# Kernel optimization log

Hardware: AMD Instinct MI355X
Metric: run time of the kernel (lower is better)

The kernel has to match this reference:

```python
import jax, jax.numpy as jnp
import numpy as np

FP8_MAX = 448.0  # torch.finfo(torch.float8_e4m3fn).max

def per_tensor_quantize(t):
    amax = jnp.max(jnp.abs(t))
    scale = FP8_MAX / jnp.maximum(amax, 1e-12)
    q = jnp.clip(t * scale, -FP8_MAX, FP8_MAX).astype(jnp.float8_e4m3fn)
    return q, (1.0 / scale).astype(jnp.float32)

def fp8_gemm(q, a_scale, w_q, w_scale, out_dtype):
    # emulate: linear(A.to(out)*a_scale, B.to(out)*b_scale)
    A = q.astype(out_dtype) * a_scale
    B = w_q.astype(out_dtype) * w_scale
    return A @ B.T

def setup_inputs() -> dict:
    key = jax.random.key(0)
    k1, k2, k3, k4 = jax.random.split(key, 4)
    tokens, hidden, ffn = 4096, 4096, 10752
    return {
        "x": jax.random.normal(k1, (tokens, hidden), jnp.float32),
        "expert_w1": jax.random.normal(k2, (ffn, hidden), jnp.float32) * 0.02,
        "expert_v1": jax.random.normal(k3, (ffn, hidden), jnp.float32) * 0.02,
        "expert_w2": jax.random.normal(k4, (ffn, hidden), jnp.float32) * 0.02,
    }

def reference(x, expert_w1, expert_v1, expert_w2):
    dt = x.dtype
    # weight quantization (as done in _quantize_weights per expert)
    w1_q, w1_s = per_tensor_quantize(expert_w1)
    v1_q, v1_s = per_tensor_quantize(expert_v1)
    w2_q, w2_s = per_tensor_quantize(expert_w2)
    # activation quantization + gate/up GEMMs
    qin, x_s = per_tensor_quantize(x)
    gate = fp8_gemm(qin, x_s, w1_q, w1_s, dt)          # [N, ffn]
    up = fp8_gemm(qin, x_s, v1_q, v1_s, dt)            # [N, ffn]
    inter = jax.nn.silu(gate) * up                      # fused GLU
    qmid, m_s = per_tensor_quantize(inter)
    # down proj uses expert_w2.t() -> B = [hidden, ffn]
    down = fp8_gemm(qmid, m_s, w2_q.T, w2_s, dt)        # [N, hidden]
    return down
```

## Files before the change

### kernel.cpp

```cpp
#include <hip/hip_runtime.h>
#include <cstdint>
#include <cstddef>

typedef float f32x4 __attribute__((ext_vector_type(4)));
typedef float f32x16 __attribute__((ext_vector_type(16)));
typedef int i32x4 __attribute__((ext_vector_type(4)));
typedef int i32x8 __attribute__((ext_vector_type(8)));
typedef unsigned char u8;

static __device__ __forceinline__ void gload_lds16(const void* g, void* l) {
  __builtin_amdgcn_global_load_lds(
      (__attribute__((address_space(1))) void*)(void*)g,
      (__attribute__((address_space(3))) void*)l,
      16, 0, 0);
}

#if defined(__has_builtin)
#if __has_builtin(__builtin_amdgcn_cvt_pk_fp8_f32)
#define HAVE_HW_FP8 1
#endif
#endif

__device__ __forceinline__ u8 f32_to_e4m3_sw(float x) {
  unsigned s = (__float_as_uint(x) >> 24) & 0x80;
  float ax = fabsf(x);
  if (!(ax > 0.0f)) return (u8)s;
  if (ax >= 448.0f) return (u8)(s | 0x7e);
  if (ax < 0.015625f) {
    int m = (int)rintf(ax * 512.0f);
    if (m >= 8) return (u8)(s | 0x08);
    return (u8)(s | m);
  }
  int e = ilogbf(ax);
  int m = (int)rintf(ldexpf(ax, 3 - e));
  if (m == 16) { ++e; m = 8; }
  return (u8)(s | ((e + 7) << 3) | (m - 8));
}

__device__ __forceinline__ unsigned cvt4_fp8(float a, float b, float c, float d) {
#ifdef HAVE_HW_FP8
  int lo = __builtin_amdgcn_cvt_pk_fp8_f32(a, b, 0, false);
  return (unsigned)__builtin_amdgcn_cvt_pk_fp8_f32(c, d, lo, true);
#else
  return (unsigned)f32_to_e4m3_sw(a) | ((unsigned)f32_to_e4m3_sw(b) << 8) |
         ((unsigned)f32_to_e4m3_sw(c) << 16) | ((unsigned)f32_to_e4m3_sw(d) << 24);
#endif
}

__global__ __launch_bounds__(256) void amax_kernel(const float* __restrict__ src, size_t n4,
                                                   unsigned* __restrict__ out) {
  float m = 0.0f;
  size_t stride = (size_t)gridDim.x * blockDim.x;
  const f32x4* p = (const f32x4*)src;
  for (size_t i = (size_t)blockIdx.x * blockDim.x + threadIdx.x; i < n4; i += stride) {
    f32x4 v = p[i];
    m = fmaxf(m, fmaxf(fmaxf(fabsf(v[0]), fabsf(v[1])), fmaxf(fabsf(v[2]), fabsf(v[3]))));
  }
#pragma unroll
  for (int off = 32; off > 0; off >>= 1) m = fmaxf(m, __shfl_down(m, off));
  __shared__ float red[4];
  int lane = threadIdx.x & 63, wid = threadIdx.x >> 6;
  if (lane == 0) red[wid] = m;
  __syncthreads();
  if (threadIdx.x == 0) {
    float v = fmaxf(fmaxf(red[0], red[1]), fmaxf(red[2], red[3]));
    atomicMax(out, __float_as_uint(v));
  }
}

__global__ __launch_bounds__(256) void quant_kernel(const float* __restrict__ src,
                                                    u8* __restrict__ dst,
                                                    const unsigned* __restrict__ amax_bits,
                                                    size_t n8) {
  float amax = __uint_as_float(*amax_bits);
  float scale = 448.0f / fmaxf(amax, 1e-12f);
  size_t stride = (size_t)gridDim.x * blockDim.x;
  const f32x4* p = (const f32x4*)src;
  uint2* q = (uint2*)dst;
  for (size_t i = (size_t)blockIdx.x * blockDim.x + threadIdx.x; i < n8; i += stride) {
    f32x4 a = p[2 * i], b = p[2 * i + 1];
    float a0 = fminf(fmaxf(a[0] * scale, -448.f), 448.f);
    float a1 = fminf(fmaxf(a[1] * scale, -448.f), 448.f);
    float a2 = fminf(fmaxf(a[2] * scale, -448.f), 448.f);
    float a3 = fminf(fmaxf(a[3] * scale, -448.f), 448.f);
    float b0 = fminf(fmaxf(b[0] * scale, -448.f), 448.f);
    float b1 = fminf(fmaxf(b[1] * scale, -448.f), 448.f);
    float b2 = fminf(fmaxf(b[2] * scale, -448.f), 448.f);
    float b3 = fminf(fmaxf(b[3] * scale, -448.f), 448.f);
    uint2 r;
    r.x = cvt4_fp8(a0, a1, a2, a3);
    r.y = cvt4_fp8(b0, b1, b2, b3);
    q[i] = r;
  }
}

__global__ __launch_bounds__(256) void quantT_kernel(const float* __restrict__ src,
                                                     u8* __restrict__ dst,
                                                     const unsigned* __restrict__ amax_bits,
                                                     int R, int C) {
  __shared__ float t[64][65];
  float amax = __uint_as_float(*amax_bits);
  float scale = 448.0f / fmaxf(amax, 1e-12f);
  int nbr = R >> 6;
  int br = (int)blockIdx.x % nbr, bc = (int)blockIdx.x / nbr;
  int r0 = br * 64, c0 = bc * 64;
  int tid = threadIdx.x;
  int lc = tid & 63, lr = tid >> 6;
#pragma unroll
  for (int i = 0; i < 16; ++i)
    t[lr + i * 4][lc] = src[(size_t)(r0 + lr + i * 4) * C + c0 + lc];
  __syncthreads();
  int qd = tid & 15, xbase = tid >> 4;
#pragma unroll
  for (int i = 0; i < 4; ++i) {
    int x = xbase + 16 * i;
    float v0 = fminf(fmaxf(t[4 * qd + 0][x] * scale, -448.f), 448.f);
    float v1 = fminf(fmaxf(t[4 * qd + 1][x] * scale, -448.f), 448.f);
    float v2 = fminf(fmaxf(t[4 * qd + 2][x] * scale, -448.f), 448.f);
    float v3 = fminf(fmaxf(t[4 * qd + 3][x] * scale, -448.f), 448.f);
    *(unsigned*)(dst + (size_t)(c0 + x) * R + r0 + 4 * qd) = cvt4_fp8(v0, v1, v2, v3);
  }
}

__device__ __forceinline__ int swz_key(int r) { return (r >> 2) & 3; }

__device__ __forceinline__ int swz_off32(int r, int h) {
  return r * 64 + ((((h << 1) ^ swz_key(r)) << 4));
}

__device__ __forceinline__ i32x8 ld_frag(const u8* base, int r, int h) {
  int o = swz_off32(r, h);
  i32x8 f;
  f.lo = *(const i32x4*)(base + o);
  f.hi = *(const i32x4*)(base + (o ^ 16));
  return f;
}

#define MFMA_MX(a, b, c) \
  __builtin_amdgcn_mfma_scale_f32_32x32x64_f8f6f4((a), (b), (c), 0, 0, 0, 0x7F7F7F7F, 0, 0x7F7F7F7F)

__global__ __launch_bounds__(256, 2) void gemm1_gateup(
    const u8* __restrict__ Aq, const u8* __restrict__ Wq, const u8* __restrict__ Vq,
    const unsigned* __restrict__ scal, float* __restrict__ inter,
    unsigned* __restrict__ amax_mid, int M, int N, int K) {
  __shared__ u8 lA[8192], lW[8192], lV[8192];
  __shared__ float red[4];
  int tid = threadIdx.x;
  int lane = tid & 63, wid = tid >> 6;
  int wm = wid >> 1, wn = wid & 1;

  int nbn = N >> 7;
  int nwg = (int)gridDim.x;
  int bid = (int)blockIdx.x;
  int cpx = nwg >> 3;
  int swz = (bid & 7) * cpx + (bid >> 3);
  int bm = swz / nbn, bn = swz - bm * nbn;

  int r0 = tid >> 2;
  int kblk = ((tid & 3) ^ swz_key(r0)) << 4;
  const u8* aS = Aq + (size_t)(bm * 128 + r0) * K + kblk;
  const u8* wS = Wq + (size_t)(bn * 128 + r0) * K + kblk;
  const u8* vS = Vq + (size_t)(bn * 128 + r0) * K + kblk;
  size_t rK = (size_t)64 * K;

  f32x16 g[2][2], u[2][2];
#pragma unroll
  for (int m = 0; m < 2; ++m)
#pragma unroll
    for (int n = 0; n < 2; ++n) {
      g[m][n] = (f32x16)(0.f);
      u[m][n] = (f32x16)(0.f);
    }

  int rfrag = lane & 31;
  int h = lane >> 5;
  int arow = wm * 64 + rfrag;
  int brow = wn * 64 + rfrag;

  for (int kt = 0; kt < K; kt += 64) {
    __syncthreads();
    gload_lds16(aS + kt, lA + tid * 16);
    gload_lds16(aS + kt + rK, lA + 4096 + tid * 16);
    gload_lds16(wS + kt, lW + tid * 16);
    gload_lds16(wS + kt + rK, lW + 4096 + tid * 16);
    gload_lds16(vS + kt, lV + tid * 16);
    gload_lds16(vS + kt + rK, lV + 4096 + tid * 16);
    __syncthreads();

    i32x8 a0 = ld_frag(lA, arow, h);
    i32x8 a1 = ld_frag(lA, arow + 32, h);
    i32x8 w0 = ld_frag(lW, brow, h);
    i32x8 w1 = ld_frag(lW, brow + 32, h);
    i32x8 v0 = ld_frag(lV, brow, h);
    i32x8 v1 = ld_frag(lV, brow + 32, h);

    g[0][0] = MFMA_MX(a0, w0, g[0][0]);
    g[0][1] = MFMA_MX(a0, w1, g[0][1]);
    g[1][0] = MFMA_MX(a1, w0, g[1][0]);
    g[1][1] = MFMA_MX(a1, w1, g[1][1]);
    u[0][0] = MFMA_MX(a0, v0, u[0][0]);
    u[0][1] = MFMA_MX(a0, v1, u[0][1]);
    u[1][0] = MFMA_MX(a1, v0, u[1][0]);
    u[1][1] = MFMA_MX(a1, v1, u[1][1]);
  }

  float ax = __uint_as_float(scal[0]);
  float aw = __uint_as_float(scal[1]);
  float av = __uint_as_float(scal[2]);
  float inv_x = 1.0f / (448.0f / fmaxf(ax, 1e-12f));
  float inv_w = 1.0f / (448.0f / fmaxf(aw, 1e-12f));
  float inv_v = 1.0f / (448.0f / fmaxf(av, 1e-12f));
  float sg = inv_x * inv_w, su = inv_x * inv_v;

  int rb = bm * 128 + wm * 64 + h * 4;
  int cb = bn * 128 + wn * 64 + rfrag;
  float lmax = 0.0f;
#pragma unroll
  for (int m = 0; m < 2; ++m)
#pragma unroll
    for (int n = 0; n < 2; ++n)
#pragma unroll
      for (int q = 0; q < 16; ++q) {
        int rr = rb + m * 32 + (q & 3) + 8 * (q >> 2);
        float gv = g[m][n][q] * sg;
        float uv = u[m][n][q] * su;
        float iv = gv / (1.0f + expf(-gv)) * uv;
        inter[(size_t)rr * N + (cb + n * 32)] = iv;
        lmax = fmaxf(lmax, fabsf(iv));
      }
#pragma unroll
  for (int off = 32; off > 0; off >>= 1) lmax = fmaxf(lmax, __shfl_down(lmax, off));
  if (lane == 0) red[wid] = lmax;
  __syncthreads();
  if (tid == 0)
    atomicMax(amax_mid, __float_as_uint(fmaxf(fmaxf(red[0], red[1]), fmaxf(red[2], red[3]))));
}

__global__ __launch_bounds__(256, 2) void gemm2_down(
    const u8* __restrict__ Aq, const u8* __restrict__ Bq,
    const unsigned* __restrict__ amax_a, const unsigned* __restrict__ amax_b,
    float* __restrict__ out, int M, int N, int K) {
  __shared__ u8 lA[8192], lB[8192];
  int tid = threadIdx.x;
  int lane = tid & 63, wid = tid >> 6;
  int wm = wid >> 1, wn = wid & 1;

  int nbn = N >> 7;
  int nwg = (int)gridDim.x;
  int bid = (int)blockIdx.x;
  int cpx = nwg >> 3;
  int swz = (bid & 7) * cpx + (bid >> 3);
  int bm = swz / nbn, bn = swz - bm * nbn;

  int r0 = tid >> 2;
  int kblk = ((tid & 3) ^ swz_key(r0)) << 4;
  const u8* aS = Aq + (size_t)(bm * 128 + r0) * K + kblk;
  const u8* bS = Bq + (size_t)(bn * 128 + r0) * K + kblk;
  size_t rK = (size_t)64 * K;

  f32x16 acc[2][2];
#pragma unroll
  for (int m = 0; m < 2; ++m)
#pragma unroll
    for (int n = 0; n < 2; ++n) acc[m][n] = (f32x16)(0.f);

  int rfrag = lane & 31;
  int h = lane >> 5;
  int arow = wm * 64 + rfrag;
  int brow = wn * 64 + rfrag;

  for (int kt = 0; kt < K; kt += 64) {
    __syncthreads();
    gload_lds16(aS + kt, lA + tid * 16);
    gload_lds16(aS + kt + rK, lA + 4096 + tid * 16);
    gload_lds16(bS + kt, lB + tid * 16);
    gload_lds16(bS + kt + rK, lB + 4096 + tid * 16);
    __syncthreads();

    i32x8 a0 = ld_frag(lA, arow, h);
    i32x8 a1 = ld_frag(lA, arow + 32, h);
    i32x8 b0 = ld_frag(lB, brow, h);
    i32x8 b1 = ld_frag(lB, brow + 32, h);

    acc[0][0] = MFMA_MX(a0, b0, acc[0][0]);
    acc[0][1] = MFMA_MX(a0, b1, acc[0][1]);
    acc[1][0] = MFMA_MX(a1, b0, acc[1][0]);
    acc[1][1] = MFMA_MX(a1, b1, acc[1][1]);
  }

  float sa = 1.0f / (448.0f / fmaxf(__uint_as_float(*amax_a), 1e-12f));
  float sb = 1.0f / (448.0f / fmaxf(__uint_as_float(*amax_b), 1e-12f));
  float sc = sa * sb;

  int rb = bm * 128 + wm * 64 + h * 4;
  int cb = bn * 128 + wn * 64 + rfrag;
#pragma unroll
  for (int m = 0; m < 2; ++m)
#pragma unroll
    for (int n = 0; n < 2; ++n)
#pragma unroll
      for (int q = 0; q < 16; ++q) {
        int rr = rb + m * 32 + (q & 3) + 8 * (q >> 2);
        out[(size_t)rr * N + (cb + n * 32)] = acc[m][n][q] * sc;
      }
}

extern "C" void kernel_launch(void* const* d_in, const int* in_sizes, int n_in,
                              void* d_out, int out_size, void* d_ws, size_t ws_size,
                              hipStream_t stream) {
  const float* x  = (const float*)d_in[0];
  const float* w1 = (const float*)d_in[1];
  const float* v1 = (const float*)d_in[2];
  const float* w2 = (const float*)d_in[3];
  const int M = 4096, H = 4096, F = 10752;

  u8* ws = (u8*)d_ws;
  unsigned* scal = (unsigned*)ws;
  u8* xq   = ws + 256;
  u8* w1q  = xq   + (size_t)M * H;
  u8* v1q  = w1q  + (size_t)F * H;
  u8* w2qT = v1q  + (size_t)F * H;
  u8* midq = w2qT + (size_t)F * H;
  float* inter = (float*)(midq + (size_t)M * F);

  hipMemsetAsync(scal, 0, 256, stream);
  amax_kernel<<<2048, 256, 0, stream>>>(x,  (size_t)M * H / 4, scal + 0);
  amax_kernel<<<2048, 256, 0, stream>>>(w1, (size_t)F * H / 4, scal + 1);
  amax_kernel<<<2048, 256, 0, stream>>>(v1, (size_t)F * H / 4, scal + 2);
  amax_kernel<<<2048, 256, 0, stream>>>(w2, (size_t)F * H / 4, scal + 3);

  quant_kernel<<<2048, 256, 0, stream>>>(x,  xq,  scal + 0, (size_t)M * H / 8);
  quant_kernel<<<2048, 256, 0, stream>>>(w1, w1q, scal + 1, (size_t)F * H / 8);
  quant_kernel<<<2048, 256, 0, stream>>>(v1, v1q, scal + 2, (size_t)F * H / 8);
  quantT_kernel<<<(F / 64) * (H / 64), 256, 0, stream>>>(w2, w2qT, scal + 3, F, H);

  gemm1_gateup<<<(M / 128) * (F / 128), 256, 0, stream>>>(xq, w1q, v1q, scal, inter,
                                                          scal + 4, M, F, H);
  quant_kernel<<<2048, 256, 0, stream>>>(inter, midq, scal + 4, (size_t)M * F / 8);
  gemm2_down<<<(M / 128) * (H / 128), 256, 0, stream>>>(midq, w2qT, scal + 4, scal + 3,
                                                        (float*)d_out, M, H, F);
}
```

Baseline: 1.059 ms.

## Triple-buffer LDS tiles with async prefetch in both FP8 GEMM kernels

```diff
diff --git a/kernel.cpp b/kernel.cpp
--- a/kernel.cpp
+++ b/kernel.cpp
@@ -143,7 +143,7 @@
     const u8* __restrict__ Aq, const u8* __restrict__ Wq, const u8* __restrict__ Vq,
     const unsigned* __restrict__ scal, float* __restrict__ inter,
     unsigned* __restrict__ amax_mid, int M, int N, int K) {
-  __shared__ u8 lA[8192], lW[8192], lV[8192];
+  __shared__ __align__(16) u8 lA[3][8192], lW[3][8192], lV[3][8192];
   __shared__ float red[4];
   int tid = threadIdx.x;
   int lane = tid & 63, wid = tid >> 6;
@@ -163,6 +163,16 @@
   const u8* vS = Vq + (size_t)(bn * 128 + r0) * K + kblk;
   size_t rK = (size_t)64 * K;
 
+#define STAGE1(buf, off)                                     \
+  do {                                                       \
+    gload_lds16(aS + (off),      lA[buf] + tid * 16);        \
+    gload_lds16(aS + (off) + rK, lA[buf] + 4096 + tid * 16); \
+    gload_lds16(wS + (off),      lW[buf] + tid * 16);        \
+    gload_lds16(wS + (off) + rK, lW[buf] + 4096 + tid * 16); \
+    gload_lds16(vS + (off),      lV[buf] + tid * 16);        \
+    gload_lds16(vS + (off) + rK, lV[buf] + 4096 + tid * 16); \
+  } while (0)
+
   f32x16 g[2][2], u[2][2];
 #pragma unroll
   for (int m = 0; m < 2; ++m)
@@ -177,23 +187,32 @@
   int arow = wm * 64 + rfrag;
   int brow = wn * 64 + rfrag;
 
-  for (int kt = 0; kt < K; kt += 64) {
-    __syncthreads();
-    gload_lds16(aS + kt, lA + tid * 16);
-    gload_lds16(aS + kt + rK, lA + 4096 + tid * 16);
-    gload_lds16(wS + kt, lW + tid * 16);
-    gload_lds16(wS + kt + rK, lW + 4096 + tid * 16);
-    gload_lds16(vS + kt, lV + tid * 16);
-    gload_lds16(vS + kt + rK, lV + 4096 + tid * 16);
-    __syncthreads();
-
-    i32x8 a0 = ld_frag(lA, arow, h);
-    i32x8 a1 = ld_frag(lA, arow + 32, h);
-    i32x8 w0 = ld_frag(lW, brow, h);
-    i32x8 w1 = ld_frag(lW, brow + 32, h);
-    i32x8 v0 = ld_frag(lV, brow, h);
-    i32x8 v1 = ld_frag(lV, brow + 32, h);
-
+  int NT = K >> 6;
+  STAGE1(0, 0);
+  STAGE1(1, 64);
+
+  for (int t = 0; t < NT; ++t) {
+    unsigned cur = (unsigned)t % 3u;
+    __builtin_amdgcn_s_barrier();
+    if (t + 2 < NT) {
+      STAGE1((cur + 2) % 3u, (t + 2) * 64);
+      asm volatile("s_waitcnt vmcnt(12)" ::: "memory");
+    } else if (t + 1 < NT) {
+      asm volatile("s_waitcnt vmcnt(6)" ::: "memory");
+    } else {
+      asm volatile("s_waitcnt vmcnt(0)" ::: "memory");
+    }
+    __builtin_amdgcn_s_barrier();
+    const u8* bA = lA[cur];
+    const u8* bW = lW[cur];
+    const u8* bV = lV[cur];
+    i32x8 a0 = ld_frag(bA, arow, h);
+    i32x8 a1 = ld_frag(bA, arow + 32, h);
+    i32x8 w0 = ld_frag(bW, brow, h);
+    i32x8 w1 = ld_frag(bW, brow + 32, h);
+    i32x8 v0 = ld_frag(bV, brow, h);
+    i32x8 v1 = ld_frag(bV, brow + 32, h);
+    __builtin_amdgcn_s_setprio(1);
     g[0][0] = MFMA_MX(a0, w0, g[0][0]);
     g[0][1] = MFMA_MX(a0, w1, g[0][1]);
     g[1][0] = MFMA_MX(a1, w0, g[1][0]);
@@ -202,7 +221,9 @@
     u[0][1] = MFMA_MX(a0, v1, u[0][1]);
     u[1][0] = MFMA_MX(a1, v0, u[1][0]);
     u[1][1] = MFMA_MX(a1, v1, u[1][1]);
-  }
+    __builtin_amdgcn_s_setprio(0);
+  }
+#undef STAGE1
 
   float ax = __uint_as_float(scal[0]);
   float aw = __uint_as_float(scal[1]);
@@ -240,7 +261,7 @@
     const u8* __restrict__ Aq, const u8* __restrict__ Bq,
     const unsigned* __restrict__ amax_a, const unsigned* __restrict__ amax_b,
     float* __restrict__ out, int M, int N, int K) {
-  __shared__ u8 lA[8192], lB[8192];
+  __shared__ __align__(16) u8 lA[3][8192], lB[3][8192];
   int tid = threadIdx.x;
   int lane = tid & 63, wid = tid >> 6;
   int wm = wid >> 1, wn = wid & 1;
@@ -258,6 +279,14 @@
   const u8* bS = Bq + (size_t)(bn * 128 + r0) * K + kblk;
   size_t rK = (size_t)64 * K;
 
+#define STAGE2(buf, off)                                     \
+  do {                                                       \
+    gload_lds16(aS + (off),      lA[buf] + tid * 16);        \
+    gload_lds16(aS + (off) + rK, lA[buf] + 4096 + tid * 16); \
+    gload_lds16(bS + (off),      lB[buf] + tid * 16);        \
+    gload_lds16(bS + (off) + rK, lB[buf] + 4096 + tid * 16); \
+  } while (0)
+
   f32x16 acc[2][2];
 #pragma unroll
   for (int m = 0; m < 2; ++m)
@@ -269,24 +298,36 @@
   int arow = wm * 64 + rfrag;
   int brow = wn * 64 + rfrag;
 
-  for (int kt = 0; kt < K; kt += 64) {
-    __syncthreads();
-    gload_lds16(aS + kt, lA + tid * 16);
-    gload_lds16(aS + kt + rK, lA + 4096 + tid * 16);
-    gload_lds16(bS + kt, lB + tid * 16);
-    gload_lds16(bS + kt + rK, lB + 4096 + tid * 16);
-    __syncthreads();
-
-    i32x8 a0 = ld_frag(lA, arow, h);
-    i32x8 a1 = ld_frag(lA, arow + 32, h);
-    i32x8 b0 = ld_frag(lB, brow, h);
-    i32x8 b1 = ld_frag(lB, brow + 32, h);
-
+  int NT = K >> 6;
+  STAGE2(0, 0);
+  STAGE2(1, 64);
+
+  for (int t = 0; t < NT; ++t) {
+    unsigned cur = (unsigned)t % 3u;
+    __builtin_amdgcn_s_barrier();
+    if (t + 2 < NT) {
+      STAGE2((cur + 2) % 3u, (t + 2) * 64);
+      asm volatile("s_waitcnt vmcnt(8)" ::: "memory");
+    } else if (t + 1 < NT) {
+      asm volatile("s_waitcnt vmcnt(4)" ::: "memory");
+    } else {
+      asm volatile("s_waitcnt vmcnt(0)" ::: "memory");
+    }
+    __builtin_amdgcn_s_barrier();
+    const u8* bA = lA[cur];
+    const u8* bB = lB[cur];
+    i32x8 a0 = ld_frag(bA, arow, h);
+    i32x8 a1 = ld_frag(bA, arow + 32, h);
+    i32x8 b0 = ld_frag(bB, brow, h);
+    i32x8 b1 = ld_frag(bB, brow + 32, h);
+    __builtin_amdgcn_s_setprio(1);
     acc[0][0] = MFMA_MX(a0, b0, acc[0][0]);
     acc[0][1] = MFMA_MX(a0, b1, acc[0][1]);
     acc[1][0] = MFMA_MX(a1, b0, acc[1][0]);
     acc[1][1] = MFMA_MX(a1, b1, acc[1][1]);
-  }
+    __builtin_amdgcn_s_setprio(0);
+  }
+#undef STAGE2
 
   float sa = 1.0f / (448.0f / fmaxf(__uint_as_float(*amax_a), 1e-12f));
   float sb = 1.0f / (448.0f / fmaxf(__uint_as_float(*amax_b), 1e-12f));
```

New measurement: 1.128 ms. +6.5%, slower.

## Use 512-thread blocks with 8 waves in both GEMMs; widen down-proj N tile

Applied to the files above, without the earlier changes.

```diff
diff --git a/kernel.cpp b/kernel.cpp
--- a/kernel.cpp
+++ b/kernel.cpp
@@ -139,15 +139,15 @@
 #define MFMA_MX(a, b, c) \
   __builtin_amdgcn_mfma_scale_f32_32x32x64_f8f6f4((a), (b), (c), 0, 0, 0, 0x7F7F7F7F, 0, 0x7F7F7F7F)
 
-__global__ __launch_bounds__(256, 2) void gemm1_gateup(
+__global__ __launch_bounds__(512, 4) void gemm1_gateup(
     const u8* __restrict__ Aq, const u8* __restrict__ Wq, const u8* __restrict__ Vq,
     const unsigned* __restrict__ scal, float* __restrict__ inter,
     unsigned* __restrict__ amax_mid, int M, int N, int K) {
-  __shared__ u8 lA[8192], lW[8192], lV[8192];
-  __shared__ float red[4];
+  __shared__ __align__(16) u8 lA[8192], lW[8192], lV[8192];
+  __shared__ float red[8];
   int tid = threadIdx.x;
   int lane = tid & 63, wid = tid >> 6;
-  int wm = wid >> 1, wn = wid & 1;
+  int wm = wid >> 2, wn = wid & 3;
 
   int nbn = N >> 7;
   int nwg = (int)gridDim.x;
@@ -161,47 +161,29 @@
   const u8* aS = Aq + (size_t)(bm * 128 + r0) * K + kblk;
   const u8* wS = Wq + (size_t)(bn * 128 + r0) * K + kblk;
   const u8* vS = Vq + (size_t)(bn * 128 + r0) * K + kblk;
-  size_t rK = (size_t)64 * K;
-
-  f32x16 g[2][2], u[2][2];
-#pragma unroll
-  for (int m = 0; m < 2; ++m)
-#pragma unroll
-    for (int n = 0; n < 2; ++n) {
-      g[m][n] = (f32x16)(0.f);
-      u[m][n] = (f32x16)(0.f);
-    }
+
+  f32x16 g0 = (f32x16)(0.f), g1 = (f32x16)(0.f);
+  f32x16 u0 = (f32x16)(0.f), u1 = (f32x16)(0.f);
 
   int rfrag = lane & 31;
   int h = lane >> 5;
   int arow = wm * 64 + rfrag;
-  int brow = wn * 64 + rfrag;
+  int wrow = wn * 32 + rfrag;
 
   for (int kt = 0; kt < K; kt += 64) {
     __syncthreads();
     gload_lds16(aS + kt, lA + tid * 16);
-    gload_lds16(aS + kt + rK, lA + 4096 + tid * 16);
     gload_lds16(wS + kt, lW + tid * 16);
-    gload_lds16(wS + kt + rK, lW + 4096 + tid * 16);
     gload_lds16(vS + kt, lV + tid * 16);
-    gload_lds16(vS + kt + rK, lV + 4096 + tid * 16);
     __syncthreads();
-
     i32x8 a0 = ld_frag(lA, arow, h);
     i32x8 a1 = ld_frag(lA, arow + 32, h);
-    i32x8 w0 = ld_frag(lW, brow, h);
-    i32x8 w1 = ld_frag(lW, brow + 32, h);
-    i32x8 v0 = ld_frag(lV, brow, h);
-    i32x8 v1 = ld_frag(lV, brow + 32, h);
-
-    g[0][0] = MFMA_MX(a0, w0, g[0][0]);
-    g[0][1] = MFMA_MX(a0, w1, g[0][1]);
-    g[1][0] = MFMA_MX(a1, w0, g[1][0]);
-    g[1][1] = MFMA_MX(a1, w1, g[1][1]);
-    u[0][0] = MFMA_MX(a0, v0, u[0][0]);
-    u[0][1] = MFMA_MX(a0, v1, u[0][1]);
-    u[1][0] = MFMA_MX(a1, v0, u[1][0]);
-    u[1][1] = MFMA_MX(a1, v1, u[1][1]);
+    i32x8 w0 = ld_frag(lW, wrow, h);
+    i32x8 v0 = ld_frag(lV, wrow, h);
+    g0 = MFMA_MX(a0, w0, g0);
+    g1 = MFMA_MX(a1, w0, g1);
+    u0 = MFMA_MX(a0, v0, u0);
+    u1 = MFMA_MX(a1, v0, u1);
   }
 
   float ax = __uint_as_float(scal[0]);
@@ -213,39 +195,44 @@
   float sg = inv_x * inv_w, su = inv_x * inv_v;
 
   int rb = bm * 128 + wm * 64 + h * 4;
-  int cb = bn * 128 + wn * 64 + rfrag;
+  int cb = bn * 128 + wn * 32 + rfrag;
   float lmax = 0.0f;
 #pragma unroll
-  for (int m = 0; m < 2; ++m)
-#pragma unroll
-    for (int n = 0; n < 2; ++n)
-#pragma unroll
-      for (int q = 0; q < 16; ++q) {
-        int rr = rb + m * 32 + (q & 3) + 8 * (q >> 2);
-        float gv = g[m][n][q] * sg;
-        float uv = u[m][n][q] * su;
-        float iv = gv / (1.0f + expf(-gv)) * uv;
-        inter[(size_t)rr * N + (cb + n * 32)] = iv;
-        lmax = fmaxf(lmax, fabsf(iv));
-      }
+  for (int mi = 0; mi < 2; ++mi) {
+    const f32x16& gg = mi ? g1 : g0;
+    const f32x16& uu = mi ? u1 : u0;
+#pragma unroll
+    for (int q = 0; q < 16; ++q) {
+      int rr = rb + mi * 32 + (q & 3) + 8 * (q >> 2);
+      float gv = gg[q] * sg;
+      float uv = uu[q] * su;
+      float iv = gv / (1.0f + expf(-gv)) * uv;
+      inter[(size_t)rr * N + cb] = iv;
+      lmax = fmaxf(lmax, fabsf(iv));
+    }
+  }
 #pragma unroll
   for (int off = 32; off > 0; off >>= 1) lmax = fmaxf(lmax, __shfl_down(lmax, off));
   if (lane == 0) red[wid] = lmax;
   __syncthreads();
-  if (tid == 0)
-    atomicMax(amax_mid, __float_as_uint(fmaxf(fmaxf(red[0], red[1]), fmaxf(red[2], red[3]))));
-}
-
-__global__ __launch_bounds__(256, 2) void gemm2_down(
+  if (tid == 0) {
+    float v = red[0];
+#pragma unroll
+    for (int i = 1; i < 8; ++i) v = fmaxf(v, red[i]);
+    atomicMax(amax_mid, __float_as_uint(v));
+  }
+}
+
+__global__ __launch_bounds__(512, 4) void gemm2_down(
     const u8* __restrict__ Aq, const u8* __restrict__ Bq,
     const unsigned* __restrict__ amax_a, const unsigned* __restrict__ amax_b,
     float* __restrict__ out, int M, int N, int K) {
-  __shared__ u8 lA[8192], lB[8192];
+  __shared__ __align__(16) u8 lA[8192], lB[16384];
   int tid = threadIdx.x;
   int lane = tid & 63, wid = tid >> 6;
-  int wm = wid >> 1, wn = wid & 1;
-
-  int nbn = N >> 7;
+  int wm = wid >> 2, wn = wid & 3;
+
+  int nbn = N >> 8;
   int nwg = (int)gridDim.x;
   int bid = (int)blockIdx.x;
   int cpx = nwg >> 3;
@@ -255,14 +242,11 @@
   int r0 = tid >> 2;
   int kblk = ((tid & 3) ^ swz_key(r0)) << 4;
   const u8* aS = Aq + (size_t)(bm * 128 + r0) * K + kblk;
-  const u8* bS = Bq + (size_t)(bn * 128 + r0) * K + kblk;
-  size_t rK = (size_t)64 * K;
-
-  f32x16 acc[2][2];
-#pragma unroll
-  for (int m = 0; m < 2; ++m)
-#pragma unroll
-    for (int n = 0; n < 2; ++n) acc[m][n] = (f32x16)(0.f);
+  const u8* bS = Bq + (size_t)(bn * 256 + r0) * K + kblk;
+  size_t rK = (size_t)128 * K;
+
+  f32x16 c00 = (f32x16)(0.f), c01 = (f32x16)(0.f);
+  f32x16 c10 = (f32x16)(0.f), c11 = (f32x16)(0.f);
 
   int rfrag = lane & 31;
   int h = lane >> 5;
@@ -272,20 +256,17 @@
   for (int kt = 0; kt < K; kt += 64) {
     __syncthreads();
     gload_lds16(aS + kt, lA + tid * 16);
-    gload_lds16(aS + kt + rK, lA + 4096 + tid * 16);
     gload_lds16(bS + kt, lB + tid * 16);
-    gload_lds16(bS + kt + rK, lB + 4096 + tid * 16);
+    gload_lds16(bS + kt + rK, lB + 8192 + tid * 16);
     __syncthreads();
-
     i32x8 a0 = ld_frag(lA, arow, h);
     i32x8 a1 = ld_frag(lA, arow + 32, h);
     i32x8 b0 = ld_frag(lB, brow, h);
     i32x8 b1 = ld_frag(lB, brow + 32, h);
-
-    acc[0][0] = MFMA_MX(a0, b0, acc[0][0]);
-    acc[0][1] = MFMA_MX(a0, b1, acc[0][1]);
-    acc[1][0] = MFMA_MX(a1, b0, acc[1][0]);
-    acc[1][1] = MFMA_MX(a1, b1, acc[1][1]);
+    c00 = MFMA_MX(a0, b0, c00);
+    c01 = MFMA_MX(a0, b1, c01);
+    c10 = MFMA_MX(a1, b0, c10);
+    c11 = MFMA_MX(a1, b1, c11);
   }
 
   float sa = 1.0f / (448.0f / fmaxf(__uint_as_float(*amax_a), 1e-12f));
@@ -293,16 +274,18 @@
   float sc = sa * sb;
 
   int rb = bm * 128 + wm * 64 + h * 4;
-  int cb = bn * 128 + wn * 64 + rfrag;
-#pragma unroll
-  for (int m = 0; m < 2; ++m)
-#pragma unroll
-    for (int n = 0; n < 2; ++n)
+  int cb = bn * 256 + wn * 64 + rfrag;
+#pragma unroll
+  for (int mi = 0; mi < 2; ++mi)
+#pragma unroll
+    for (int ni = 0; ni < 2; ++ni) {
+      const f32x16& cc = mi ? (ni ? c11 : c10) : (ni ? c01 : c00);
 #pragma unroll
       for (int q = 0; q < 16; ++q) {
-        int rr = rb + m * 32 + (q & 3) + 8 * (q >> 2);
-        out[(size_t)rr * N + (cb + n * 32)] = acc[m][n][q] * sc;
+        int rr = rb + mi * 32 + (q & 3) + 8 * (q >> 2);
+        out[(size_t)rr * N + (cb + ni * 32)] = cc[q] * sc;
       }
+    }
 }
 
 extern "C" void kernel_launch(void* const* d_in, const int* in_sizes, int n_in,
@@ -334,9 +317,9 @@
   quant_kernel<<<2048, 256, 0, stream>>>(v1, v1q, scal + 2, (size_t)F * H / 8);
   quantT_kernel<<<(F / 64) * (H / 64), 256, 0, stream>>>(w2, w2qT, scal + 3, F, H);
 
-  gemm1_gateup<<<(M / 128) * (F / 128), 256, 0, stream>>>(xq, w1q, v1q, scal, inter,
+  gemm1_gateup<<<(M / 128) * (F / 128), 512, 0, stream>>>(xq, w1q, v1q, scal, inter,
                                                           scal + 4, M, F, H);
   quant_kernel<<<2048, 256, 0, stream>>>(inter, midq, scal + 4, (size_t)M * F / 8);
-  gemm2_down<<<(M / 128) * (H / 128), 256, 0, stream>>>(midq, w2qT, scal + 4, scal + 3,
+  gemm2_down<<<(M / 128) * (H / 256), 512, 0, stream>>>(midq, w2qT, scal + 4, scal + 3,
                                                         (float*)d_out, M, H, F);
 }
```

Measured after the change: 1.018 ms. 3.9% less time.
